# Performance work log

Measured on AMD Instinct MI355X. Metric: run time of the kernel, lower is better.

The kernel has to match this reference:

```python
import jax, jax.numpy as jnp
import numpy as np

B, T, D = 64, 1024, 512
H, O = 512, 128
HALF = D // 2
ALPHA_M = 0.8


def setup_inputs() -> dict:
    key = jax.random.key(0)
    ks = jax.random.split(key, 6)
    s_in = 1.0 / np.sqrt(HALF)
    s_h = 1.0 / np.sqrt(H)
    return {
        "x": jax.random.normal(ks[0], (B, T, D), dtype=jnp.float32),
        "w1": jax.random.uniform(ks[1], (H, HALF), jnp.float32, -s_in, s_in),
        "b1": jnp.zeros((H,), jnp.float32),
        "tau1": jnp.full((H,), 3.0, jnp.float32),
        "w2": jax.random.uniform(ks[2], (H, HALF), jnp.float32, -s_in, s_in),
        "b2": jnp.zeros((H,), jnp.float32),
        "tau2": jnp.full((H,), 0.5, jnp.float32),
        "wo": jax.random.uniform(ks[3], (O, H), jnp.float32, -s_h, s_h),
        "bo": jnp.zeros((O,), jnp.float32),
    }


def reference(x, w1, b1, tau1, w2, b2, tau2, wo, bo):
    # Hoist the per-timestep branch Linears into two batched GEMMs.
    d1_in = jnp.einsum("bti,hi->tbh", x[:, :, :HALF], w1) + b1  # [T,B,H]
    d2_in = jnp.einsum("bti,hi->tbh", x[:, :, HALF:], w2) + b2  # [T,B,H]

    a1 = jax.nn.sigmoid(tau1)  # [H]
    a2 = jax.nn.sigmoid(tau2)  # [H]

    def step(carry, ins):
        d1, d2, mem = carry
        i1, i2 = ins
        d1 = a1 * d1 + (1.0 - a1) * i1
        d2 = a2 * d2 + (1.0 - a2) * i2
        mem = ALPHA_M * mem + (1.0 - ALPHA_M) * (d1 + d2)
        return (d1, d2, mem), mem

    z = jnp.zeros((x.shape[0], tau1.shape[0]), x.dtype)
    _, mems = jax.lax.scan(step, (z, z, z), (d1_in, d2_in))  # mems: [T,B,H]

    # Output projection + sigmoid, vectorized over all timesteps.
    out = jax.nn.sigmoid(jnp.einsum("tbh,oh->bto", mems, wo) + bo)  # [B,T,O]
    return out
```

## Files before the change

### kernel.cpp

```cpp
#include <hip/hip_runtime.h>


#define B_    64
#define T_    1024
#define D_    512
#define H_    512
#define O_    128
#define HALF_ 256
#define CLEN  32
#define NC    32

typedef __attribute__((ext_vector_type(4))) float        f32x4;
typedef __attribute__((ext_vector_type(2))) float        f32x2;
typedef __attribute__((ext_vector_type(8))) short        s16x8;
typedef __attribute__((ext_vector_type(4))) unsigned int u32x4;
typedef __attribute__((ext_vector_type(2))) unsigned int u32x2;

__device__ __forceinline__ unsigned short f2bf(float f) {
    unsigned u = __float_as_uint(f);
    return (unsigned short)((u + 0x7fffu + ((u >> 16) & 1u)) >> 16);
}
__device__ __forceinline__ unsigned packbf(float a, float b) {
    return (unsigned)f2bf(a) | ((unsigned)f2bf(b) << 16);
}
__device__ __forceinline__ float bflo(unsigned u) { return __uint_as_float(u << 16); }
__device__ __forceinline__ float bfhi(unsigned u) { return __uint_as_float(u & 0xffff0000u); }
__device__ __forceinline__ float sigf(float x) { return 1.f / (1.f + __expf(-x)); }
__device__ __forceinline__ float guard(float dn) {
    if (fabsf(dn) < 1e-6f) dn = (dn < 0.f ? -1e-6f : 1e-6f);
    return dn;
}
__device__ __forceinline__ float pw32(float a) {
    float t = a * a; t *= t; t *= t; t *= t; t *= t; return t;
}

typedef const __attribute__((address_space(1))) unsigned int gu32;
typedef __attribute__((address_space(3))) unsigned int      lu32;
__device__ __forceinline__ void gl_lds16(const void* g, void* l) {
    __builtin_amdgcn_global_load_lds((gu32*)g, (lu32*)l, 16, 0, 0);
}

__global__ __launch_bounds__(256) void gtab_kernel(
    const float* __restrict__ tau1, const float* __restrict__ tau2,
    float* __restrict__ G1, float* __restrict__ G2)
{
    const int h = blockIdx.x * 256 + threadIdx.x;
    const float a1 = sigf(tau1[h]), a2 = sigf(tau2[h]);
    const float c1 = 0.2f * a1 / guard(0.8f - a1);
    const float c2 = 0.2f * a2 / guard(0.8f - a2);
    float pm = 1.f, p1 = 1.f, p2 = 1.f;
    for (int k = 0; k < CLEN; ++k) {
        pm *= 0.8f; p1 *= a1; p2 *= a2;
        G1[k * H_ + h] = c1 * (pm - p1);
        G2[k * H_ + h] = c2 * (pm - p2);
    }
}

__global__ __launch_bounds__(256) void wcast_kernel(
    const float* __restrict__ w1, const float* __restrict__ w2,
    const float* __restrict__ wo,
    unsigned int* __restrict__ w1b, unsigned int* __restrict__ w2b,
    unsigned int* __restrict__ wob)
{
    const float* s; unsigned int* d; int n;
    if (blockIdx.y == 0)      { s = w1; d = w1b; n = H_ * HALF_; }
    else if (blockIdx.y == 1) { s = w2; d = w2b; n = H_ * HALF_; }
    else                      { s = wo; d = wob; n = O_ * H_;    }
    int i = (blockIdx.x * 256 + threadIdx.x) * 4;
    if (i >= n) return;
    f32x4 a = *(const f32x4*)(s + i);
    u32x2 p;
    p.x = packbf(a.x, a.y);
    p.y = packbf(a.z, a.w);
    *(u32x2*)(d + i / 2) = p;
}

__global__ __launch_bounds__(256) void cast_kernel(const float* __restrict__ x,
                                                   unsigned int* __restrict__ xb) {
    size_t i = ((size_t)blockIdx.x * 256 + threadIdx.x) * 8;
    f32x4 a = *(const f32x4*)(x + i);
    f32x4 b = *(const f32x4*)(x + i + 4);
    u32x4 p;
    p.x = packbf(a.x, a.y); p.y = packbf(a.z, a.w);
    p.z = packbf(b.x, b.y); p.w = packbf(b.z, b.w);
    *(u32x4*)(xb + i / 2) = p;
}

__global__ __launch_bounds__(256, 2) void gemm1f_kernel(
    const unsigned short* __restrict__ xb,
    const unsigned short* __restrict__ w1b, const unsigned short* __restrict__ w2b,
    const float* __restrict__ b1, const float* __restrict__ tau1,
    const float* __restrict__ b2, const float* __restrict__ tau2,
    unsigned int* __restrict__ mems,
    float* __restrict__ Sd1, float* __restrict__ Sd2, float* __restrict__ Sm)
{
    __shared__ short smem[32768];
    short* As  = smem;
    short* Bs  = smem + 8192;
    short* d1L = smem + 16384;
    short* d2L = smem;

    const int nt = blockIdx.x;
    const int mt = blockIdx.y;
    const int b  = mt >> 3;
    const int t0 = (mt & 7) << 7;

    const int tid = threadIdx.x, l = tid & 63, wv = tid >> 6;
    const int ln = l & 15, qd = l >> 4;
    const int wm = (wv & 1) << 6, wn = (wv >> 1) << 6;

    for (int br = 0; br < 2; ++br) {
        const unsigned short* wb = br ? w2b : w1b;
        const unsigned short* abase = xb + (size_t)(mt * 128) * D_ + br * HALF_;
        const unsigned short* wbase = wb + (size_t)(nt * 128) * HALF_;

        f32x4 acc[4][4] = {};

        for (int kt = 0; kt < HALF_; kt += 64) {
            #pragma unroll
            for (int i = 0; i < 4; ++i) {
                int ch = wv * 4 + i;
                int r  = ch * 8 + (l >> 3);
                int kbl = (l & 7) ^ (r & 7);
                gl_lds16(abase + (size_t)r * D_ + kt + kbl * 8, &As[ch * 512 + l * 8]);
            }
            #pragma unroll
            for (int i = 0; i < 4; ++i) {
                int ch = wv * 4 + i;
                int r  = ch * 8 + (l >> 3);
                int kbl = (l & 7) ^ (r & 7);
                gl_lds16(wbase + (size_t)r * HALF_ + kt + kbl * 8, &Bs[ch * 512 + l * 8]);
            }
            __syncthreads();
            #pragma unroll
            for (int ks = 0; ks < 64; ks += 32) {
                s16x8 af[4], bfv[4];
                #pragma unroll
                for (int i = 0; i < 4; ++i) {
                    int r = wm + i * 16 + ln;
                    int kbp = ((ks >> 3) + qd) ^ (r & 7);
                    af[i] = *(const s16x8*)&As[r * 64 + kbp * 8];
                }
                #pragma unroll
                for (int j = 0; j < 4; ++j) {
                    int r = wn + j * 16 + ln;
                    int kbp = ((ks >> 3) + qd) ^ (r & 7);
                    bfv[j] = *(const s16x8*)&Bs[r * 64 + kbp * 8];
                }
                #pragma unroll
                for (int i = 0; i < 4; ++i)
                    #pragma unroll
                    for (int j = 0; j < 4; ++j)
                        acc[i][j] = __builtin_amdgcn_mfma_f32_16x16x32_bf16(
                            af[i], bfv[j], acc[i][j], 0, 0, 0);
            }
            __syncthreads();
        }

        short* dL = br ? d2L : d1L;
        #pragma unroll
        for (int i = 0; i < 4; ++i)
            #pragma unroll
            for (int j = 0; j < 4; ++j)
                #pragma unroll
                for (int r = 0; r < 4; ++r)
                    dL[(wm + i * 16 + qd * 4 + r) * 128 + wn + j * 16 + ln] =
                        (short)f2bf(acc[i][j][r]);
    }
    __syncthreads();

    const int cl  = tid >> 6;
    const int h2l = tid & 63;
    const int hl0 = h2l << 1;
    const int hg0 = nt * 128 + hl0;
    const int cg  = ((mt & 7) << 2) + cl;

    const float a1a = sigf(tau1[hg0]), a1b = sigf(tau1[hg0 + 1]);
    const float a2a = sigf(tau2[hg0]), a2b = sigf(tau2[hg0 + 1]);
    const float o1a = 1.f - a1a, o1b = 1.f - a1b;
    const float o2a = 1.f - a2a, o2b = 1.f - a2b;
    const float bb1a = b1[hg0], bb1b = b1[hg0 + 1];
    const float bb2a = b2[hg0], bb2b = b2[hg0 + 1];

    float d1a = 0.f, d1b = 0.f, d2a = 0.f, d2b = 0.f, ma = 0.f, mb = 0.f;
    const size_t mrow = (size_t)(b * T_ + t0 + cl * CLEN) * (H_ / 2) + nt * 64 + h2l;

    #pragma unroll 8
    for (int k = 0; k < CLEN; ++k) {
        unsigned u1 = *(const unsigned*)&d1L[(cl * CLEN + k) * 128 + hl0];
        unsigned u2 = *(const unsigned*)&d2L[(cl * CLEN + k) * 128 + hl0];
        float i1a = bflo(u1) + bb1a, i1b = bfhi(u1) + bb1b;
        float i2a = bflo(u2) + bb2a, i2b = bfhi(u2) + bb2b;
        d1a = a1a * d1a + o1a * i1a;  d1b = a1b * d1b + o1b * i1b;
        d2a = a2a * d2a + o2a * i2a;  d2b = a2b * d2b + o2b * i2b;
        ma = 0.8f * ma + 0.2f * (d1a + d2a);
        mb = 0.8f * mb + 0.2f * (d1b + d2b);
        mems[mrow + (size_t)k * (H_ / 2)] = packbf(ma, mb);
    }

    const size_t si = (size_t)(cg * B_ + b) * H_ + hg0;
    f32x2 v;
    v.x = d1a; v.y = d1b; *(f32x2*)&Sd1[si] = v;
    v.x = d2a; v.y = d2b; *(f32x2*)&Sd2[si] = v;
    v.x = ma;  v.y = mb;  *(f32x2*)&Sm[si]  = v;
}

__global__ __launch_bounds__(128) void scanB_kernel(
    const float* __restrict__ Sd1, const float* __restrict__ Sd2,
    const float* __restrict__ Sm,
    const float* __restrict__ tau1, const float* __restrict__ tau2,
    float* __restrict__ D1, float* __restrict__ D2, float* __restrict__ DM)
{
    const int g = blockIdx.x * 128 + threadIdx.x;
    const int h2 = g & 255, b = g >> 8, h0 = h2 << 1;

    const float a1a = sigf(tau1[h0]), a1b = sigf(tau1[h0 + 1]);
    const float a2a = sigf(tau2[h0]), a2b = sigf(tau2[h0 + 1]);
    const float amL = pw32(0.8f);
    const float a1La = pw32(a1a), a1Lb = pw32(a1b);
    const float a2La = pw32(a2a), a2Lb = pw32(a2b);

    const float c1a = 0.2f * a1a / guard(0.8f - a1a);
    const float c1b = 0.2f * a1b / guard(0.8f - a1b);
    const float c2a = 0.2f * a2a / guard(0.8f - a2a);
    const float c2b = 0.2f * a2b / guard(0.8f - a2b);

    const float g1La = c1a * (amL - a1La), g1Lb = c1b * (amL - a1Lb);
    const float g2La = c2a * (amL - a2La), g2Lb = c2b * (amL - a2Lb);

    float D1a = 0.f, D1b = 0.f, D2a = 0.f, D2b = 0.f, Ma = 0.f, Mb = 0.f;
    for (int c = 0; c < NC; ++c) {
        const size_t si = (size_t)(c * B_ + b) * H_ + h0;
        f32x2 v;
        v.x = D1a; v.y = D1b; *(f32x2*)&D1[si] = v;
        v.x = D2a; v.y = D2b; *(f32x2*)&D2[si] = v;
        v.x = Ma;  v.y = Mb;  *(f32x2*)&DM[si] = v;
        f32x2 s1 = *(const f32x2*)&Sd1[si];
        f32x2 s2 = *(const f32x2*)&Sd2[si];
        f32x2 sm = *(const f32x2*)&Sm[si];
        float nMa = amL * Ma + D1a * g1La + D2a * g2La + sm.x;
        float nMb = amL * Mb + D1b * g1Lb + D2b * g2Lb + sm.y;
        D1a = a1La * D1a + s1.x;  D1b = a1Lb * D1b + s1.y;
        D2a = a2La * D2a + s2.x;  D2b = a2Lb * D2b + s2.y;
        Ma = nMa;  Mb = nMb;
    }
}

__global__ __launch_bounds__(256, 2) void gemm2f_kernel(
    const unsigned short* __restrict__ mems, const unsigned short* __restrict__ wob,
    const float* __restrict__ bo,
    const float* __restrict__ G1, const float* __restrict__ G2,
    const float* __restrict__ D1, const float* __restrict__ D2,
    const float* __restrict__ DM, float* __restrict__ out)
{
    __shared__ short As[128 * 64];
    __shared__ short Bs[128 * 64];
    __shared__ float PMl[CLEN];

    const int mt = blockIdx.x;
    const int b = mt >> 3, c0 = (mt & 7) << 2;
    const int tid = threadIdx.x, l = tid & 63, wv = tid >> 6;
    const int ln = l & 15, qd = l >> 4;
    const int wm = (wv & 1) << 6, wn = (wv >> 1) << 6;

    if (tid < CLEN) {
        float pm = 1.f;
        for (int k = 0; k <= tid; ++k) pm *= 0.8f;
        PMl[tid] = pm;
    }
    __syncthreads();

    f32x4 acc[4][4] = {};
    const unsigned short* abase = mems + (size_t)(mt * 128) * H_;

    for (int kt = 0; kt < H_; kt += 64) {
        #pragma unroll
        for (int i = 0; i < 4; ++i) {
            int ch = wv * 4 + i;
            int r  = ch * 8 + (l >> 3);
            int kbl = (l & 7) ^ (r & 7);
            gl_lds16(wob + (size_t)r * H_ + kt + kbl * 8, &Bs[ch * 512 + l * 8]);
        }
        #pragma unroll
        for (int i = 0; i < 4; ++i) {
            int gi = i * 256 + tid;
            int r = gi >> 3, kbp = gi & 7, kbl = kbp ^ (r & 7);
            int h0 = kt + kbl * 8;
            int k = r & 31, c = c0 + (r >> 5);
            size_t dbase = (size_t)(c * B_ + b) * H_ + h0;
            f32x4 d1a = *(const f32x4*)&D1[dbase], d1b = *(const f32x4*)&D1[dbase + 4];
            f32x4 d2a = *(const f32x4*)&D2[dbase], d2b = *(const f32x4*)&D2[dbase + 4];
            f32x4 dma = *(const f32x4*)&DM[dbase], dmb = *(const f32x4*)&DM[dbase + 4];
            f32x4 g1a = *(const f32x4*)&G1[k * H_ + h0], g1b = *(const f32x4*)&G1[k * H_ + h0 + 4];
            f32x4 g2a = *(const f32x4*)&G2[k * H_ + h0], g2b = *(const f32x4*)&G2[k * H_ + h0 + 4];
            float pm = PMl[k];
            u32x4 mv = *(const u32x4*)(abase + (size_t)r * H_ + h0);
            float v0 = bflo(mv.x) + d1a.x * g1a.x + d2a.x * g2a.x + dma.x * pm;
            float v1 = bfhi(mv.x) + d1a.y * g1a.y + d2a.y * g2a.y + dma.y * pm;
            float v2 = bflo(mv.y) + d1a.z * g1a.z + d2a.z * g2a.z + dma.z * pm;
            float v3 = bfhi(mv.y) + d1a.w * g1a.w + d2a.w * g2a.w + dma.w * pm;
            float v4 = bflo(mv.z) + d1b.x * g1b.x + d2b.x * g2b.x + dmb.x * pm;
            float v5 = bfhi(mv.z) + d1b.y * g1b.y + d2b.y * g2b.y + dmb.y * pm;
            float v6 = bflo(mv.w) + d1b.z * g1b.z + d2b.z * g2b.z + dmb.z * pm;
            float v7 = bfhi(mv.w) + d1b.w * g1b.w + d2b.w * g2b.w + dmb.w * pm;
            u32x4 p;
            p.x = packbf(v0, v1); p.y = packbf(v2, v3);
            p.z = packbf(v4, v5); p.w = packbf(v6, v7);
            *(u32x4*)&As[r * 64 + kbp * 8] = p;
        }
        __syncthreads();
        #pragma unroll
        for (int ks = 0; ks < 64; ks += 32) {
            s16x8 af[4], bfv[4];
            #pragma unroll
            for (int i = 0; i < 4; ++i) {
                int r = wm + i * 16 + ln;
                int kbp = ((ks >> 3) + qd) ^ (r & 7);
                af[i] = *(const s16x8*)&As[r * 64 + kbp * 8];
            }
            #pragma unroll
            for (int j = 0; j < 4; ++j) {
                int r = wn + j * 16 + ln;
                int kbp = ((ks >> 3) + qd) ^ (r & 7);
                bfv[j] = *(const s16x8*)&Bs[r * 64 + kbp * 8];
            }
            #pragma unroll
            for (int i = 0; i < 4; ++i)
                #pragma unroll
                for (int j = 0; j < 4; ++j)
                    acc[i][j] = __builtin_amdgcn_mfma_f32_16x16x32_bf16(
                        af[i], bfv[j], acc[i][j], 0, 0, 0);
        }
        __syncthreads();
    }

    float bov[4];
    #pragma unroll
    for (int j = 0; j < 4; ++j) bov[j] = bo[wn + j * 16 + ln];

    float* orow = out + (size_t)(mt * 128 + wm + qd * 4) * O_ + wn + ln;
    #pragma unroll
    for (int i = 0; i < 4; ++i)
        #pragma unroll
        for (int j = 0; j < 4; ++j)
            #pragma unroll
            for (int r = 0; r < 4; ++r) {
                float v = acc[i][j][r] + bov[j];
                orow[(size_t)(i * 16 + r) * O_ + j * 16] = 1.f / (1.f + __expf(-v));
            }
}

extern "C" void kernel_launch(void* const* d_in, const int* in_sizes, int n_in,
                              void* d_out, int out_size, void* d_ws, size_t ws_size,
                              hipStream_t stream) {
    const float* x    = (const float*)d_in[0];
    const float* w1   = (const float*)d_in[1];
    const float* b1   = (const float*)d_in[2];
    const float* tau1 = (const float*)d_in[3];
    const float* w2   = (const float*)d_in[4];
    const float* b2   = (const float*)d_in[5];
    const float* tau2 = (const float*)d_in[6];
    const float* wo   = (const float*)d_in[7];
    const float* bo   = (const float*)d_in[8];
    float* out = (float*)d_out;

    char* w = (char*)d_ws;
    unsigned short* xb   = (unsigned short*)(w);
    unsigned int*   mems = (unsigned int*)(w + (size_t)64 * 1024 * 1024);
    float* Sd1 = (float*)(w + (size_t)128 * 1024 * 1024);
    float* Sd2 = Sd1 + (1u << 20);
    float* Sm  = Sd1 + (2u << 20);
    float* D1  = Sd1 + (3u << 20);
    float* D2  = Sd1 + (4u << 20);
    float* DM  = Sd1 + (5u << 20);
    float* G1  = Sd1 + (6u << 20);
    float* G2  = G1 + CLEN * H_;
    unsigned short* w1b = (unsigned short*)(G2 + CLEN * H_);
    unsigned short* w2b = w1b + (size_t)H_ * HALF_;
    unsigned short* wob = w2b + (size_t)H_ * HALF_;

    gtab_kernel<<<dim3(2), 256, 0, stream>>>(tau1, tau2, G1, G2);
    wcast_kernel<<<dim3(128, 3), 256, 0, stream>>>(w1, w2, wo,
                                                   (unsigned int*)w1b,
                                                   (unsigned int*)w2b,
                                                   (unsigned int*)wob);
    cast_kernel<<<dim3(16384), 256, 0, stream>>>(x, (unsigned int*)xb);
    gemm1f_kernel<<<dim3(4, 512), 256, 0, stream>>>(xb, w1b, w2b, b1, tau1, b2, tau2,
                                                    mems, Sd1, Sd2, Sm);
    scanB_kernel<<<dim3(128), 128, 0, stream>>>(Sd1, Sd2, Sm, tau1, tau2, D1, D2, DM);
    gemm2f_kernel<<<dim3(512), 256, 0, stream>>>((const unsigned short*)mems, wob, bo,
                                                 G1, G2, D1, D2, DM, out);
}
```

Measured before the change: 359.3 us.

## Compute both branch GEMMs in one K loop with swizzled LDS epilogue

Merges the two sequential branch GEMM passes into one K loop that stages the x halves and both weight tiles into LDS together and keeps two accumulator sets live. This halves the number of K-loop barriers and gives each wave more independent MFMA work per sync. The LDS epilogue now XOR-swizzles the column index by time row to cut bank conflicts on the transposed writes and scan reads. The cost is twice the accumulator registers, which may lower occupancy under the launch bound of 2 blocks per SM, and the full 64KB of LDS in use.

Result: no change. 362.1 us (+0.8%).

```diff
diff --git a/kernel.cpp b/kernel.cpp
--- a/kernel.cpp
+++ b/kernel.cpp
@@ -95,10 +95,12 @@
     float* __restrict__ Sd1, float* __restrict__ Sd2, float* __restrict__ Sm)
 {
     __shared__ short smem[32768];
-    short* As  = smem;
-    short* Bs  = smem + 8192;
-    short* d1L = smem + 16384;
-    short* d2L = smem;
+    short* As1 = smem;
+    short* As2 = smem + 8192;
+    short* Bs1 = smem + 16384;
+    short* Bs2 = smem + 24576;
+    short* d1L = smem;
+    short* d2L = smem + 16384;
 
     const int nt = blockIdx.x;
     const int mt = blockIdx.y;
@@ -109,64 +111,97 @@
     const int ln = l & 15, qd = l >> 4;
     const int wm = (wv & 1) << 6, wn = (wv >> 1) << 6;
 
-    for (int br = 0; br < 2; ++br) {
-        const unsigned short* wb = br ? w2b : w1b;
-        const unsigned short* abase = xb + (size_t)(mt * 128) * D_ + br * HALF_;
-        const unsigned short* wbase = wb + (size_t)(nt * 128) * HALF_;
-
-        f32x4 acc[4][4] = {};
-
-        for (int kt = 0; kt < HALF_; kt += 64) {
+    const unsigned short* abase  = xb + (size_t)(mt * 128) * D_;
+    const unsigned short* w1base = w1b + (size_t)(nt * 128) * HALF_;
+    const unsigned short* w2base = w2b + (size_t)(nt * 128) * HALF_;
+
+    f32x4 acc0[4][4] = {};
+    f32x4 acc1[4][4] = {};
+
+    for (int kt = 0; kt < HALF_; kt += 64) {
+        #pragma unroll
+        for (int i = 0; i < 4; ++i) {
+            int ch = wv * 4 + i;
+            int r  = ch * 8 + (l >> 3);
+            int kbl = (l & 7) ^ (r & 7);
+            gl_lds16(abase + (size_t)r * D_ + kt + kbl * 8,         &As1[ch * 512 + l * 8]);
+        }
+        #pragma unroll
+        for (int i = 0; i < 4; ++i) {
+            int ch = wv * 4 + i;
+            int r  = ch * 8 + (l >> 3);
+            int kbl = (l & 7) ^ (r & 7);
+            gl_lds16(abase + (size_t)r * D_ + HALF_ + kt + kbl * 8, &As2[ch * 512 + l * 8]);
+        }
+        #pragma unroll
+        for (int i = 0; i < 4; ++i) {
+            int ch = wv * 4 + i;
+            int r  = ch * 8 + (l >> 3);
+            int kbl = (l & 7) ^ (r & 7);
+            gl_lds16(w1base + (size_t)r * HALF_ + kt + kbl * 8,     &Bs1[ch * 512 + l * 8]);
+        }
+        #pragma unroll
+        for (int i = 0; i < 4; ++i) {
+            int ch = wv * 4 + i;
+            int r  = ch * 8 + (l >> 3);
+            int kbl = (l & 7) ^ (r & 7);
+            gl_lds16(w2base + (size_t)r * HALF_ + kt + kbl * 8,     &Bs2[ch * 512 + l * 8]);
+        }
+        __syncthreads();
+        #pragma unroll
+        for (int ks = 0; ks < 64; ks += 32) {
+            s16x8 af[4], bfv[4];
             #pragma unroll
             for (int i = 0; i < 4; ++i) {
-                int ch = wv * 4 + i;
-                int r  = ch * 8 + (l >> 3);
-                int kbl = (l & 7) ^ (r & 7);
-                gl_lds16(abase + (size_t)r * D_ + kt + kbl * 8, &As[ch * 512 + l * 8]);
-            }
+                int r = wm + i * 16 + ln;
+                int kbp = ((ks >> 3) + qd) ^ (r & 7);
+                af[i] = *(const s16x8*)&As1[r * 64 + kbp * 8];
+            }
+            #pragma unroll
+            for (int j = 0; j < 4; ++j) {
+                int r = wn + j * 16 + ln;
+                int kbp = ((ks >> 3) + qd) ^ (r & 7);
+                bfv[j] = *(const s16x8*)&Bs1[r * 64 + kbp * 8];
+            }
+            #pragma unroll
+            for (int i = 0; i < 4; ++i)
+                #pragma unroll
+                for (int j = 0; j < 4; ++j)
+                    acc0[i][j] = __builtin_amdgcn_mfma_f32_16x16x32_bf16(
+                        af[i], bfv[j], acc0[i][j], 0, 0, 0);
             #pragma unroll
             for (int i = 0; i < 4; ++i) {
-                int ch = wv * 4 + i;
-                int r  = ch * 8 + (l >> 3);
-                int kbl = (l & 7) ^ (r & 7);
-                gl_lds16(wbase + (size_t)r * HALF_ + kt + kbl * 8, &Bs[ch * 512 + l * 8]);
-            }
-            __syncthreads();
-            #pragma unroll
-            for (int ks = 0; ks < 64; ks += 32) {
-                s16x8 af[4], bfv[4];
+                int r = wm + i * 16 + ln;
+                int kbp = ((ks >> 3) + qd) ^ (r & 7);
+                af[i] = *(const s16x8*)&As2[r * 64 + kbp * 8];
+            }
+            #pragma unroll
+            for (int j = 0; j < 4; ++j) {
+                int r = wn + j * 16 + ln;
+                int kbp = ((ks >> 3) + qd) ^ (r & 7);
+                bfv[j] = *(const s16x8*)&Bs2[r * 64 + kbp * 8];
+            }
+            #pragma unroll
+            for (int i = 0; i < 4; ++i)
                 #pragma unroll
-                for (int i = 0; i < 4; ++i) {
-                    int r = wm + i * 16 + ln;
-                    int kbp = ((ks >> 3) + qd) ^ (r & 7);
-                    af[i] = *(const s16x8*)&As[r * 64 + kbp * 8];
-                }
-                #pragma unroll
-                for (int j = 0; j < 4; ++j) {
-                    int r = wn + j * 16 + ln;
-                    int kbp = ((ks >> 3) + qd) ^ (r & 7);
-                    bfv[j] = *(const s16x8*)&Bs[r * 64 + kbp * 8];
-                }
-                #pragma unroll
-                for (int i = 0; i < 4; ++i)
-                    #pragma unroll
-                    for (int j = 0; j < 4; ++j)
-                        acc[i][j] = __builtin_amdgcn_mfma_f32_16x16x32_bf16(
-                            af[i], bfv[j], acc[i][j], 0, 0, 0);
-            }
-            __syncthreads();
-        }
-
-        short* dL = br ? d2L : d1L;
-        #pragma unroll
-        for (int i = 0; i < 4; ++i)
-            #pragma unroll
-            for (int j = 0; j < 4; ++j)
-                #pragma unroll
-                for (int r = 0; r < 4; ++r)
-                    dL[(wm + i * 16 + qd * 4 + r) * 128 + wn + j * 16 + ln] =
-                        (short)f2bf(acc[i][j][r]);
-    }
+                for (int j = 0; j < 4; ++j)
+                    acc1[i][j] = __builtin_amdgcn_mfma_f32_16x16x32_bf16(
+                        af[i], bfv[j], acc1[i][j], 0, 0, 0);
+        }
+        __syncthreads();
+    }
+
+    #pragma unroll
+    for (int i = 0; i < 4; ++i)
+        #pragma unroll
+        for (int j = 0; j < 4; ++j)
+            #pragma unroll
+            for (int r = 0; r < 4; ++r) {
+                int t  = wm + i * 16 + qd * 4 + r;
+                int hc = (wn + j * 16 + ln) ^ ((t & 12) << 2);
+                d1L[t * 128 + hc] = (short)f2bf(acc0[i][j][r]);
+                d2L[t * 128 + hc] = (short)f2bf(acc1[i][j][r]);
+            }
     __syncthreads();
 
     const int cl  = tid >> 6;
@@ -187,8 +222,10 @@
 
     #pragma unroll 8
     for (int k = 0; k < CLEN; ++k) {
-        unsigned u1 = *(const unsigned*)&d1L[(cl * CLEN + k) * 128 + hl0];
-        unsigned u2 = *(const unsigned*)&d2L[(cl * CLEN + k) * 128 + hl0];
+        int t  = cl * CLEN + k;
+        int hc = hl0 ^ ((t & 12) << 2);
+        unsigned u1 = *(const unsigned*)&d1L[t * 128 + hc];
+        unsigned u2 = *(const unsigned*)&d2L[t * 128 + hc];
         float i1a = bflo(u1) + bb1a, i1b = bfhi(u1) + bb1b;
         float i2a = bflo(u2) + bb2a, i2b = bfhi(u2) + bb2b;
         d1a = a1a * d1a + o1a * i1a;  d1b = a1b * d1b + o1b * i1b;
```
